# Optimization experiments

Measured on AMD Instinct MI355X. Metric: run time of the kernel, lower is better.

## Reference

```python
import jax, jax.numpy as jnp
import numpy as np
from jax import lax

NMS_THRESHOLD = 0.45
PRE_THRESHOLD = 0.005


def setup_inputs() -> dict:
    key = jax.random.key(0)
    k1, k2 = jax.random.split(key)
    B, C, N = 8, 20, 2048
    u = jax.random.uniform(k1, (B, N, 4), dtype=jnp.float32)  # raw rand per spec
    # build valid [x1,y1,x2,y2] boxes from raw uniforms (center + size param)
    cx, cy = u[..., 0], u[..., 1]
    w = u[..., 2] * 0.2 + 0.01
    h = u[..., 3] * 0.2 + 0.01
    bbs = jnp.stack([cx - w / 2, cy - h / 2, cx + w / 2, cy + h / 2], axis=-1)
    conf = jax.random.uniform(k2, (B, C, N), dtype=jnp.float32)
    return {"bbs": bbs, "conf": conf}


def _nms_filter(bbs, conf, nms_threshold, pre_threshold):
    # bbs: [B, N, 4] (x1,y1,x2,y2); conf: [B, C, N]
    B, C, N = conf.shape
    order = jnp.argsort(-conf, axis=-1)                      # [B,C,N] desc by score
    conf_s = jnp.take_along_axis(conf, order, axis=-1)       # sorted scores
    boxes_b = jnp.broadcast_to(bbs[:, None, :, :], (B, C, N, 4))
    boxes_s = jnp.take_along_axis(boxes_b, order[..., None], axis=2)  # [B,C,N,4]

    x1, y1, x2, y2 = (boxes_s[..., i] for i in range(4))
    areas = jnp.maximum(x2 - x1, 0.0) * jnp.maximum(y2 - y1, 0.0)     # [B,C,N]
    pos = jnp.arange(N)

    keep0 = conf_s > pre_threshold  # pre-threshold: dropped boxes never kept nor suppress

    def body(i, keep):
        # box at sorted rank i
        bx1 = lax.dynamic_index_in_dim(x1, i, 2, keepdims=True)  # [B,C,1]
        by1 = lax.dynamic_index_in_dim(y1, i, 2, keepdims=True)
        bx2 = lax.dynamic_index_in_dim(x2, i, 2, keepdims=True)
        by2 = lax.dynamic_index_in_dim(y2, i, 2, keepdims=True)
        a_i = lax.dynamic_index_in_dim(areas, i, 2, keepdims=True)
        iw = jnp.maximum(jnp.minimum(bx2, x2) - jnp.maximum(bx1, x1), 0.0)
        ih = jnp.maximum(jnp.minimum(by2, y2) - jnp.maximum(by1, y1), 0.0)
        inter = iw * ih
        iou = inter / jnp.maximum(a_i + areas - inter, 1e-12)    # [B,C,N]
        keep_i = lax.dynamic_index_in_dim(keep, i, 2, keepdims=True)  # alive pivot?
        suppress = (iou > nms_threshold) & (pos > i) & keep_i
        return keep & ~suppress

    keep = lax.fori_loop(0, N, body, keep0)
    filt_s = conf_s * keep.astype(conf_s.dtype)
    inv = jnp.argsort(order, axis=-1)                          # inverse permutation
    return jnp.take_along_axis(filt_s, inv, axis=-1)


def reference(bbs, conf):
    return _nms_filter(bbs, conf, NMS_THRESHOLD, PRE_THRESHOLD)
```

## Files before the change

### kernel.cpp

```cpp
#include <hip/hip_runtime.h>


#define BB   8
#define CC   20
#define NBOX 2048
#define CAP  64
#define PRE_THR 0.005f
#define IOU_M 0x1.CCCCCDp-2

typedef unsigned long long u64;
typedef unsigned int u32;
typedef unsigned short u16;

__device__ __forceinline__ float area_rn(float x1, float y1, float x2, float y2) {
    return __fmul_rn(fmaxf(__fsub_rn(x2, x1), 0.f), fmaxf(__fsub_rn(y2, y1), 0.f));
}
__device__ __forceinline__ bool iou_gt(float inter, float den) {
    return (double)inter > IOU_M * (double)den;
}

__global__ __launch_bounds__(1024) void adj_kernel(const float4* __restrict__ bbs,
                                                   u32* __restrict__ deg,
                                                   u16* __restrict__ nbr) {
    const int batch = blockIdx.x >> 5;
    const int seg   = blockIdx.x & 31;
    const int lane  = threadIdx.x & 63;
    const int wv    = threadIdx.x >> 6;

    __shared__ float4 sbox[NBOX];
    __shared__ float  sar[NBOX];

    const float4* bp = bbs + (size_t)batch * NBOX;
    for (int n = threadIdx.x; n < NBOX; n += 1024) {
        float4 bv = bp[n];
        sbox[n] = bv;
        sar[n]  = area_rn(bv.x, bv.y, bv.z, bv.w);
    }
    __syncthreads();

    const int r0 = seg * 64 + wv * 4;
    float4 rb[4]; float ra[4]; u32 hits[4] = {0, 0, 0, 0};
    #pragma unroll
    for (int t = 0; t < 4; ++t) { rb[t] = sbox[r0 + t]; ra[t] = sar[r0 + t]; }

    #pragma unroll 4
    for (int k = 0; k < 32; ++k) {
        const int c = lane + (k << 6);
        const float4 cb = sbox[c];
        const float  ca = sar[c];
        #pragma unroll
        for (int t = 0; t < 4; ++t) {
            float iw = fmaxf(__fsub_rn(fminf(rb[t].z, cb.z), fmaxf(rb[t].x, cb.x)), 0.f);
            float ih = fmaxf(__fsub_rn(fminf(rb[t].w, cb.w), fmaxf(rb[t].y, cb.y)), 0.f);
            float inter = __fmul_rn(iw, ih);
            float den = fmaxf(__fsub_rn(__fadd_rn(ra[t], ca), inter), 1e-12f);
            if (c != r0 + t && iou_gt(inter, den)) hits[t] |= 1u << k;
        }
    }

    #pragma unroll
    for (int t = 0; t < 4; ++t) {
        const int i = r0 + t;
        int cnt = __popc(hits[t]);
        int ofs = cnt;
        #pragma unroll
        for (int d = 1; d < 64; d <<= 1) {
            int v = __shfl_up(ofs, d);
            if (lane >= d) ofs += v;
        }
        int total = __shfl(ofs, 63);
        ofs -= cnt;
        u16* row = nbr + ((size_t)batch * NBOX + i) * CAP;
        u32 h = hits[t];
        while (h) {
            int k = __ffs(h) - 1; h &= h - 1;
            if (ofs < CAP) row[ofs] = (u16)(lane + (k << 6));
            ++ofs;
        }
        if (lane == 0) deg[batch * NBOX + i] = (u32)min(total, CAP);
    }
}

__global__ __launch_bounds__(256) void prop_kernel(const float* __restrict__ conf,
                                                   const u32* __restrict__ deg,
                                                   const u16* __restrict__ nbr,
                                                   float* __restrict__ out) {
    const int wg   = blockIdx.x;
    const int b    = wg / CC;
    const int base = wg * NBOX;
    const int tid  = threadIdx.x;

    __shared__ u64           skey[NBOX];
    __shared__ unsigned char sstate[NBOX];
    __shared__ int sflag;

    const u32* degb = deg + b * NBOX;
    const u16* nbrb = nbr + (size_t)b * NBOX * CAP;

    float cv[8]; u32 dreg[8]; u32 und = 0;
    #pragma unroll
    for (int p = 0; p < 8; ++p) {
        const int i = tid + (p << 8);
        float c = conf[base + i];
        cv[p] = c;
        dreg[p] = degb[i];
        skey[i] = ((u64)__float_as_uint(c) << 32) | (u32)(~i);
        bool live = (c > PRE_THR);
        sstate[i] = live ? 0 : 2;
        if (live) und |= 1u << p;
    }
    if (tid == 0) sflag = 0;
    __syncthreads();

    while (true) {
        bool changed = false;
        u32 m = und;
        while (m) {
            const int p = __ffs(m) - 1; m &= m - 1;
            const int i = tid + (p << 8);
            const u64 ki = skey[i];
            const int d  = (int)dreg[p];
            const u16* row = nbrb + (size_t)i * CAP;
            int verdict = 1;
            for (int e = 0; e < d; ++e) {
                const int j = row[e];
                if (skey[j] > ki) {
                    const int st = sstate[j];
                    if (st == 1) { verdict = 2; break; }
                    if (st == 0) verdict = 0;
                }
            }
            if (verdict != 0) {
                sstate[i] = (unsigned char)verdict;
                und &= ~(1u << p);
                changed = true;
            }
        }
        if (changed) sflag = 1;
        __syncthreads();
        const int f = sflag;
        __syncthreads();
        if (!f) break;
        if (tid == 0) sflag = 0;
        __syncthreads();
    }

    #pragma unroll
    for (int p = 0; p < 8; ++p) {
        const int i = tid + (p << 8);
        out[base + i] = (sstate[i] == 1) ? cv[p] : 0.f;
    }
}

#define NMS_THR 0.45f
__global__ __launch_bounds__(256) void nms_mono(const float* __restrict__ bbs,
                                                const float* __restrict__ conf,
                                                float* __restrict__ out) {
    const int wg   = blockIdx.x;
    const int b    = wg / CC;
    const int base = wg * NBOX;
    const int tid  = threadIdx.x;
    const int lane = tid & 63;
    const int wv   = tid >> 6;

    __shared__ union {
        u64 keys[NBOX];
        struct { float x1[NBOX], y1[NBOX], x2[NBOX], y2[NBOX]; } a;
    } u;
    __shared__ u64           Mcol[NBOX];
    __shared__ int           sidx[NBOX];
    __shared__ unsigned char skeep[NBOX];

    for (int n = tid; n < NBOX; n += 256) {
        float cvv = conf[base + n];
        u.keys[n] = ((u64)__float_as_uint(cvv) << 32) | (u32)(~n);
    }
    __syncthreads();
    for (int k = 2; k <= NBOX; k <<= 1)
        for (int j = k >> 1; j > 0; j >>= 1) {
            const int mask = j - 1;
            for (int t = tid; t < NBOX / 2; t += 256) {
                int i = ((t & ~mask) << 1) | (t & mask), ip = i + j;
                u64 a = u.keys[i], c2 = u.keys[ip];
                if ((a < c2) == ((i & k) == 0)) { u.keys[i] = c2; u.keys[ip] = a; }
            }
            __syncthreads();
        }
    u64 myk[8];
    #pragma unroll
    for (int p = 0; p < 8; ++p) myk[p] = u.keys[tid + p * 256];
    __syncthreads();
    #pragma unroll
    for (int p = 0; p < 8; ++p) {
        int r = tid + p * 256;
        u64 key = myk[p];
        int idx = (int)(~(u32)key) & (NBOX - 1);
        float cvv = __uint_as_float((u32)(key >> 32));
        float4 bv = ((const float4*)bbs)[b * NBOX + idx];
        u.a.x1[r] = bv.x; u.a.y1[r] = bv.y; u.a.x2[r] = bv.z; u.a.y2[r] = bv.w;
        sidx[r] = idx;
        skeep[r] = (cvv > PRE_THR) ? 1 : 0;
        out[base + idx] = cvv;
    }
    __syncthreads();
    for (int c = wv; c < NBOX / 64; c += 4) {
        int r = c * 64 + lane;
        float bx1 = u.a.x1[r], by1 = u.a.y1[r], bx2 = u.a.x2[r], by2 = u.a.y2[r];
        float bar = area_rn(bx1, by1, bx2, by2);
        u64 col = 0;
        for (int s = 1; s < 64; ++s) {
            int src = (lane + s) & 63;
            float px1 = __shfl(bx1, src), py1 = __shfl(by1, src);
            float px2 = __shfl(bx2, src), py2 = __shfl(by2, src);
            float par = area_rn(px1, py1, px2, py2);
            float iw = fmaxf(__fsub_rn(fminf(px2, bx2), fmaxf(px1, bx1)), 0.f);
            float ih = fmaxf(__fsub_rn(fminf(py2, by2), fmaxf(py1, by1)), 0.f);
            float inter = __fmul_rn(iw, ih);
            float den = fmaxf(__fsub_rn(__fadd_rn(bar, par), inter), 1e-12f);
            if ((__fdiv_rn(inter, den) > NMS_THR) && (src > lane)) col |= 1ull << src;
        }
        Mcol[r] = col;
    }
    __syncthreads();
    for (int cb = 0; cb < NBOX; cb += 64) {
        bool k0 = skeep[cb + lane] != 0;
        u64 alive = __ballot(k0);
        if (alive)
            for (int l = 0; l < 64; ++l) {
                u64 cl = Mcol[cb + l];
                u64 take = (u64)0 - ((alive >> l) & 1ull);
                alive &= ~(cl & take);
            }
        if (tid < 64) skeep[cb + lane] = (unsigned char)((alive >> lane) & 1ull);
        if (alive)
            for (int jb = cb + 64 + wv * 64; jb < NBOX; jb += 256) {
                int jj = jb + lane;
                bool jk = skeep[jj] != 0;
                if (__ballot(jk)) {
                    float jx1 = u.a.x1[jj], jy1 = u.a.y1[jj];
                    float jx2 = u.a.x2[jj], jy2 = u.a.y2[jj];
                    float jar = area_rn(jx1, jy1, jx2, jy2);
                    bool dead = false;
                    u64 m = alive;
                    while (m) {
                        int l = __ffsll(m) - 1; m &= m - 1;
                        int r = cb + l;
                        float px1 = u.a.x1[r], py1 = u.a.y1[r];
                        float px2 = u.a.x2[r], py2 = u.a.y2[r];
                        float par = area_rn(px1, py1, px2, py2);
                        float iw = fmaxf(__fsub_rn(fminf(px2, jx2), fmaxf(px1, jx1)), 0.f);
                        float ih = fmaxf(__fsub_rn(fminf(py2, jy2), fmaxf(py1, jy1)), 0.f);
                        float inter = __fmul_rn(iw, ih);
                        float den = fmaxf(__fsub_rn(__fadd_rn(par, jar), inter), 1e-12f);
                        dead = dead | (__fdiv_rn(inter, den) > NMS_THR);
                    }
                    if (jk && dead) skeep[jj] = 0;
                }
            }
        __syncthreads();
    }
    #pragma unroll
    for (int p = 0; p < 8; ++p) {
        int r = tid + p * 256;
        if (!skeep[r]) out[base + sidx[r]] = 0.0f;
    }
}

extern "C" void kernel_launch(void* const* d_in, const int* in_sizes, int n_in,
                              void* d_out, int out_size, void* d_ws, size_t ws_size,
                              hipStream_t stream) {
    const float* bbs  = (const float*)d_in[0];
    const float* conf = (const float*)d_in[1];
    float* out = (float*)d_out;

    const size_t deg_bytes = (size_t)BB * NBOX * sizeof(u32);
    const size_t nbr_bytes = (size_t)BB * NBOX * CAP * sizeof(u16);
    if (ws_size >= deg_bytes + nbr_bytes) {
        u32* deg = (u32*)d_ws;
        u16* nbr = (u16*)((char*)d_ws + deg_bytes);
        adj_kernel<<<dim3(BB * 32), dim3(1024), 0, stream>>>((const float4*)bbs, deg, nbr);
        prop_kernel<<<dim3(BB * CC), dim3(256), 0, stream>>>(conf, deg, nbr, out);
    } else {
        nms_mono<<<dim3(BB * CC), dim3(256), 0, stream>>>(bbs, conf, out);
    }
}
```

Before: 109.8 us.

## Compact higher-score neighbor edges into shared memory before NMS propagation

The propagation kernel now prefilters each box's neighbor list, keeping only live neighbors with higher score (ties broken by index). Using a block-wide prefix scan, it packs these edges into a shared-memory array so the iterative fixed-point loop reads compact LDS edge lists instead of global neighbor rows with key comparisons. Boxes with no such neighbors are marked kept right away, and each sync round now performs two local sweeps. If the compacted edges exceed the shared capacity it falls back to the old global-memory path. The cost is an extra pass over global neighbor rows and a larger shared-memory footprint.

New measurement: 129.5 us. +17.9%, slower.

```diff
diff --git a/kernel.cpp b/kernel.cpp
--- a/kernel.cpp
+++ b/kernel.cpp
@@ -5,6 +5,7 @@
 #define CC   20
 #define NBOX 2048
 #define CAP  64
+#define MAXE 20480
 #define PRE_THR 0.005f
 #define IOU_M 0x1.CCCCCDp-2
 
@@ -89,60 +90,157 @@
     const int b    = wg / CC;
     const int base = wg * NBOX;
     const int tid  = threadIdx.x;
-
-    __shared__ u64           skey[NBOX];
-    __shared__ unsigned char sstate[NBOX];
+    const int lane = tid & 63;
+    const int wv   = tid >> 6;
+
+    __shared__ float          sconf[NBOX];
+    __shared__ unsigned char  sstate[NBOX];
+    __shared__ union { u16 edge[MAXE]; u64 skey[NBOX]; } e;
+    __shared__ int wtot[4];
     __shared__ int sflag;
 
     const u32* degb = deg + b * NBOX;
     const u16* nbrb = nbr + (size_t)b * NBOX * CAP;
 
-    float cv[8]; u32 dreg[8]; u32 und = 0;
+    float cv[8]; int dreg[8];
     #pragma unroll
     for (int p = 0; p < 8; ++p) {
         const int i = tid + (p << 8);
         float c = conf[base + i];
         cv[p] = c;
-        dreg[p] = degb[i];
-        skey[i] = ((u64)__float_as_uint(c) << 32) | (u32)(~i);
-        bool live = (c > PRE_THR);
-        sstate[i] = live ? 0 : 2;
-        if (live) und |= 1u << p;
+        sconf[i] = c;
+        dreg[p] = (int)degb[i];
+        sstate[i] = (c > PRE_THR) ? 0 : 2;
     }
     if (tid == 0) sflag = 0;
     __syncthreads();
 
-    while (true) {
-        bool changed = false;
-        u32 m = und;
-        while (m) {
-            const int p = __ffs(m) - 1; m &= m - 1;
+    int hcnt[8]; u32 und = 0;
+    #pragma unroll
+    for (int p = 0; p < 8; ++p) {
+        const int i = tid + (p << 8);
+        int cnt = 0;
+        if (sstate[i] == 0) {
+            const u32 bi = __float_as_uint(cv[p]);
+            const u16* row = nbrb + (size_t)i * CAP;
+            for (int k = 0; k < dreg[p]; ++k) {
+                const int j = row[k];
+                if (sstate[j] != 2) {
+                    const u32 bj = __float_as_uint(sconf[j]);
+                    if (bj > bi || (bj == bi && j < i)) ++cnt;
+                }
+            }
+            if (cnt == 0) sstate[i] = 1;
+            else und |= 1u << p;
+        }
+        hcnt[p] = cnt;
+    }
+
+    int tsum = 0;
+    #pragma unroll
+    for (int p = 0; p < 8; ++p) tsum += hcnt[p];
+    int incl = tsum;
+    #pragma unroll
+    for (int d = 1; d < 64; d <<= 1) {
+        int v = __shfl_up(incl, d);
+        if (lane >= d) incl += v;
+    }
+    if (lane == 63) wtot[wv] = incl;
+    __syncthreads();
+    int wbase = 0;
+    for (int w = 0; w < wv; ++w) wbase += wtot[w];
+    const int total = wtot[0] + wtot[1] + wtot[2] + wtot[3];
+    int tbase = wbase + incl - tsum;
+
+    if (total <= MAXE) {
+        int soff[8];
+        #pragma unroll
+        for (int p = 0; p < 8; ++p) {
+            soff[p] = tbase;
+            if (hcnt[p]) {
+                const int i = tid + (p << 8);
+                const u32 bi = __float_as_uint(cv[p]);
+                const u16* row = nbrb + (size_t)i * CAP;
+                for (int k = 0; k < dreg[p]; ++k) {
+                    const int j = row[k];
+                    if (sstate[j] != 2) {
+                        const u32 bj = __float_as_uint(sconf[j]);
+                        if (bj > bi || (bj == bi && j < i)) e.edge[tbase++] = (u16)j;
+                    }
+                }
+            }
+        }
+        __syncthreads();
+
+        while (true) {
+            bool changed = false;
+            #pragma unroll 1
+            for (int it = 0; it < 2; ++it) {
+                u32 m = und;
+                while (m) {
+                    const int p = __ffs(m) - 1; m &= m - 1;
+                    const int i = tid + (p << 8);
+                    bool any_alive = false, any_pend = false;
+                    const int o = soff[p], n = hcnt[p];
+                    for (int k = 0; k < n; ++k) {
+                        const int st = sstate[e.edge[o + k]];
+                        any_alive |= (st == 1);
+                        any_pend  |= (st == 0);
+                        if (any_alive) break;
+                    }
+                    if (any_alive || !any_pend) {
+                        sstate[i] = any_alive ? 2 : 1;
+                        und &= ~(1u << p);
+                        changed = true;
+                    }
+                }
+            }
+            if (changed) sflag = 1;
+            __syncthreads();
+            const int f = sflag;
+            __syncthreads();
+            if (!f) break;
+            if (tid == 0) sflag = 0;
+            __syncthreads();
+        }
+    } else {
+        #pragma unroll
+        for (int p = 0; p < 8; ++p) {
             const int i = tid + (p << 8);
-            const u64 ki = skey[i];
-            const int d  = (int)dreg[p];
-            const u16* row = nbrb + (size_t)i * CAP;
-            int verdict = 1;
-            for (int e = 0; e < d; ++e) {
-                const int j = row[e];
-                if (skey[j] > ki) {
-                    const int st = sstate[j];
-                    if (st == 1) { verdict = 2; break; }
-                    if (st == 0) verdict = 0;
-                }
-            }
-            if (verdict != 0) {
-                sstate[i] = (unsigned char)verdict;
-                und &= ~(1u << p);
-                changed = true;
-            }
-        }
-        if (changed) sflag = 1;
+            e.skey[i] = ((u64)__float_as_uint(cv[p]) << 32) | (u32)(~i);
+        }
         __syncthreads();
-        const int f = sflag;
-        __syncthreads();
-        if (!f) break;
-        if (tid == 0) sflag = 0;
-        __syncthreads();
+        while (true) {
+            bool changed = false;
+            u32 m = und;
+            while (m) {
+                const int p = __ffs(m) - 1; m &= m - 1;
+                const int i = tid + (p << 8);
+                const u64 ki = e.skey[i];
+                const u16* row = nbrb + (size_t)i * CAP;
+                int verdict = 1;
+                for (int k = 0; k < dreg[p]; ++k) {
+                    const int j = row[k];
+                    if (e.skey[j] > ki) {
+                        const int st = sstate[j];
+                        if (st == 1) { verdict = 2; break; }
+                        if (st == 0) verdict = 0;
+                    }
+                }
+                if (verdict != 0) {
+                    sstate[i] = (unsigned char)verdict;
+                    und &= ~(1u << p);
+                    changed = true;
+                }
+            }
+            if (changed) sflag = 1;
+            __syncthreads();
+            const int f = sflag;
+            __syncthreads();
+            if (!f) break;
+            if (tid == 0) sflag = 0;
+            __syncthreads();
+        }
     }
 
     #pragma unroll
```

## Precompute per-box higher-score neighbor lists in registers for NMS propagation

Applied to the files above, without the earlier changes.

The adjacency kernel now also writes a compact 8-entry neighbor copy per box. The propagation kernel loads it with one 16-byte read, filters once to the neighbors that outrank the box and are above the pre-threshold, and packs up to 8 of them into registers. Later fixed-point sweeps then check only those packed indices against shared state instead of re-reading global neighbor rows and 64-bit keys. Boxes with more than 8 dominating neighbors fall back to the full-row scan. This adds more register pressure and an extra workspace buffer.

Result: slower. 112.5 us (+2.4%).

```diff
diff --git a/kernel.cpp b/kernel.cpp
--- a/kernel.cpp
+++ b/kernel.cpp
@@ -21,7 +21,8 @@
 
 __global__ __launch_bounds__(1024) void adj_kernel(const float4* __restrict__ bbs,
                                                    u32* __restrict__ deg,
-                                                   u16* __restrict__ nbr) {
+                                                   u16* __restrict__ nbr,
+                                                   u16* __restrict__ nbr8) {
     const int batch = blockIdx.x >> 5;
     const int seg   = blockIdx.x & 31;
     const int lane  = threadIdx.x & 63;
@@ -70,11 +71,14 @@
         }
         int total = __shfl(ofs, 63);
         ofs -= cnt;
-        u16* row = nbr + ((size_t)batch * NBOX + i) * CAP;
+        u16* row  = nbr  + ((size_t)batch * NBOX + i) * CAP;
+        u16* row8 = nbr8 + ((size_t)batch * NBOX + i) * 8;
         u32 h = hits[t];
         while (h) {
             int k = __ffs(h) - 1; h &= h - 1;
-            if (ofs < CAP) row[ofs] = (u16)(lane + (k << 6));
+            u16 j = (u16)(lane + (k << 6));
+            if (ofs < 8)   row8[ofs] = j;
+            if (ofs < CAP) row[ofs]  = j;
             ++ofs;
         }
         if (lane == 0) deg[batch * NBOX + i] = (u32)min(total, CAP);
@@ -84,56 +88,136 @@
 __global__ __launch_bounds__(256) void prop_kernel(const float* __restrict__ conf,
                                                    const u32* __restrict__ deg,
                                                    const u16* __restrict__ nbr,
+                                                   const u16* __restrict__ nbr8,
                                                    float* __restrict__ out) {
     const int wg   = blockIdx.x;
     const int b    = wg / CC;
     const int base = wg * NBOX;
     const int tid  = threadIdx.x;
 
-    __shared__ u64           skey[NBOX];
+    __shared__ float         sconf[NBOX];
     __shared__ unsigned char sstate[NBOX];
     __shared__ int sflag;
 
-    const u32* degb = deg + b * NBOX;
-    const u16* nbrb = nbr + (size_t)b * NBOX * CAP;
-
-    float cv[8]; u32 dreg[8]; u32 und = 0;
+    const u32*   degb = deg  + b * NBOX;
+    const u16*   nbrb = nbr  + (size_t)b * NBOX * CAP;
+    const uint4* n8b  = (const uint4*)nbr8 + (size_t)b * NBOX;
+
+    float cv[8]; int dreg[8]; uint4 nv[8];
     #pragma unroll
     for (int p = 0; p < 8; ++p) {
         const int i = tid + (p << 8);
-        float c = conf[base + i];
-        cv[p] = c;
-        dreg[p] = degb[i];
-        skey[i] = ((u64)__float_as_uint(c) << 32) | (u32)(~i);
-        bool live = (c > PRE_THR);
-        sstate[i] = live ? 0 : 2;
-        if (live) und |= 1u << p;
+        cv[p]   = conf[base + i];
+        dreg[p] = (int)degb[i];
+        nv[p]   = n8b[i];
+    }
+    #pragma unroll
+    for (int p = 0; p < 8; ++p) {
+        const int i = tid + (p << 8);
+        sconf[i]  = cv[p];
+        sstate[i] = (cv[p] > PRE_THR) ? 0 : 2;
     }
     if (tid == 0) sflag = 0;
+    __syncthreads();
+
+    u64 h0[8], h1[8]; u32 vm[8];
+    u32 und = 0, slow = 0;
+    #pragma unroll
+    for (int p = 0; p < 8; ++p) {
+        h0[p] = 0; h1[p] = 0;
+        const int i = tid + (p << 8);
+        int cnt = 0;
+        if (sstate[i] == 0) {
+            const u32 bi = __float_as_uint(cv[p]);
+            const int d  = dreg[p];
+            const u32 w[4] = { nv[p].x, nv[p].y, nv[p].z, nv[p].w };
+            #pragma unroll
+            for (int k = 0; k < 8; ++k) {
+                if (k < d) {
+                    const int j = (int)((w[k >> 1] >> ((k & 1) << 4)) & 0xffff);
+                    if (sstate[j] != 2) {
+                        const u32 bj = __float_as_uint(sconf[j]);
+                        if (bj > bi || (bj == bi && j < i)) {
+                            if (cnt < 4)      h0[p] |= (u64)j << (cnt << 4);
+                            else if (cnt < 8) h1[p] |= (u64)j << ((cnt - 4) << 4);
+                            ++cnt;
+                        }
+                    }
+                }
+            }
+            if (d > 8) {
+                const u16* row = nbrb + (size_t)i * CAP;
+                for (int k = 8; k < d; ++k) {
+                    const int j = row[k];
+                    if (sstate[j] != 2) {
+                        const u32 bj = __float_as_uint(sconf[j]);
+                        if (bj > bi || (bj == bi && j < i)) {
+                            if (cnt < 4)      h0[p] |= (u64)j << (cnt << 4);
+                            else if (cnt < 8) h1[p] |= (u64)j << ((cnt - 4) << 4);
+                            ++cnt;
+                        }
+                    }
+                }
+            }
+            if (cnt == 0) sstate[i] = 1;
+            else {
+                und |= 1u << p;
+                if (cnt > 8) slow |= 1u << p;
+            }
+        }
+        vm[p] = (cnt >= 8) ? 0xffu : ((1u << cnt) - 1u);
+    }
     __syncthreads();
 
     while (true) {
         bool changed = false;
-        u32 m = und;
-        while (m) {
-            const int p = __ffs(m) - 1; m &= m - 1;
-            const int i = tid + (p << 8);
-            const u64 ki = skey[i];
-            const int d  = (int)dreg[p];
-            const u16* row = nbrb + (size_t)i * CAP;
-            int verdict = 1;
-            for (int e = 0; e < d; ++e) {
-                const int j = row[e];
-                if (skey[j] > ki) {
-                    const int st = sstate[j];
-                    if (st == 1) { verdict = 2; break; }
-                    if (st == 0) verdict = 0;
+        #pragma unroll 1
+        for (int sweep = 0; sweep < 2; ++sweep) {
+            #pragma unroll
+            for (int p = 0; p < 8; ++p) {
+                if (und & (1u << p)) {
+                    const int i = tid + (p << 8);
+                    if (!(slow & (1u << p))) {
+                        u32 alive_b = 0, pend_b = 0;
+                        #pragma unroll
+                        for (int k = 0; k < 4; ++k) {
+                            const int j = (int)((h0[p] >> (k << 4)) & 0xffff);
+                            const int st = sstate[j];
+                            alive_b |= (u32)(st == 1) << k;
+                            pend_b  |= (u32)(st == 0) << k;
+                        }
+                        #pragma unroll
+                        for (int k = 0; k < 4; ++k) {
+                            const int j = (int)((h1[p] >> (k << 4)) & 0xffff);
+                            const int st = sstate[j];
+                            alive_b |= (u32)(st == 1) << (k + 4);
+                            pend_b  |= (u32)(st == 0) << (k + 4);
+                        }
+                        if (alive_b & vm[p]) {
+                            sstate[i] = 2; und &= ~(1u << p); changed = true;
+                        } else if (!(pend_b & vm[p])) {
+                            sstate[i] = 1; und &= ~(1u << p); changed = true;
+                        }
+                    } else {
+                        const u32 bi = __float_as_uint(cv[p]);
+                        const u16* row = nbrb + (size_t)i * CAP;
+                        int verdict = 1;
+                        for (int k = 0; k < dreg[p]; ++k) {
+                            const int j = row[k];
+                            const int st = sstate[j];
+                            if (st == 2) continue;
+                            const u32 bj = __float_as_uint(sconf[j]);
+                            if (bj > bi || (bj == bi && j < i)) {
+                                if (st == 1) { verdict = 2; break; }
+                                verdict = 0;
+                            }
+                        }
+                        if (verdict != 0) {
+                            sstate[i] = (unsigned char)verdict;
+                            und &= ~(1u << p); changed = true;
+                        }
+                    }
                 }
-            }
-            if (verdict != 0) {
-                sstate[i] = (unsigned char)verdict;
-                und &= ~(1u << p);
-                changed = true;
             }
         }
         if (changed) sflag = 1;
@@ -273,13 +357,15 @@
     const float* conf = (const float*)d_in[1];
     float* out = (float*)d_out;
 
-    const size_t deg_bytes = (size_t)BB * NBOX * sizeof(u32);
-    const size_t nbr_bytes = (size_t)BB * NBOX * CAP * sizeof(u16);
-    if (ws_size >= deg_bytes + nbr_bytes) {
-        u32* deg = (u32*)d_ws;
-        u16* nbr = (u16*)((char*)d_ws + deg_bytes);
-        adj_kernel<<<dim3(BB * 32), dim3(1024), 0, stream>>>((const float4*)bbs, deg, nbr);
-        prop_kernel<<<dim3(BB * CC), dim3(256), 0, stream>>>(conf, deg, nbr, out);
+    const size_t deg_bytes  = (size_t)BB * NBOX * sizeof(u32);
+    const size_t nbr_bytes  = (size_t)BB * NBOX * CAP * sizeof(u16);
+    const size_t nbr8_bytes = (size_t)BB * NBOX * 8 * sizeof(u16);
+    if (ws_size >= deg_bytes + nbr_bytes + nbr8_bytes) {
+        u32* deg  = (u32*)d_ws;
+        u16* nbr  = (u16*)((char*)d_ws + deg_bytes);
+        u16* nbr8 = (u16*)((char*)d_ws + deg_bytes + nbr_bytes);
+        adj_kernel<<<dim3(BB * 32), dim3(1024), 0, stream>>>((const float4*)bbs, deg, nbr, nbr8);
+        prop_kernel<<<dim3(BB * CC), dim3(256), 0, stream>>>(conf, deg, nbr, nbr8, out);
     } else {
         nms_mono<<<dim3(BB * CC), dim3(256), 0, stream>>>(bbs, conf, out);
     }
```
